# Kernel optimization log

Hardware: AMD Instinct MI355X
Metric: run time of the kernel (lower is better)

## Reference

```python
import jax, jax.numpy as jnp
import numpy as np

STRIDE = 14
C_LOCAL = 2
NUM_HEADS = 12


def sparse_attention_mask(n_tokens, stride_length=STRIDE, c=C_LOCAL, mode='fixed'):
    q = jnp.arange(n_tokens)[:, None]  # row index Q
    k = jnp.arange(n_tokens)[None, :]  # col index K
    if mode == 'fixed':
        m1 = (q // stride_length) == (k // stride_length)
        m2 = ((k % stride_length) >= stride_length - c) & ((k % stride_length) <= stride_length)
        return m1 | m2
    elif mode == 'strided':
        m1 = jnp.abs(q - k) <= stride_length
        m2 = ((q - k) % stride_length) == 0
        return m1 | m2


def setup_inputs() -> dict:
    key = jax.random.key(0)
    ks = jax.random.split(key, 5)
    B, N, C = 16, 1024, 768
    return {
        'x': jax.random.normal(ks[0], (B, N, C), dtype=jnp.float32),
        'w_qkv': jax.random.normal(ks[1], (3 * C, C), dtype=jnp.float32) * (1.0 / np.sqrt(C)),
        'b_qkv': jax.random.normal(ks[2], (3 * C,), dtype=jnp.float32) * 0.02,
        'w_proj': jax.random.normal(ks[3], (C, C), dtype=jnp.float32) * (1.0 / np.sqrt(C)),
        'b_proj': jax.random.normal(ks[4], (C,), dtype=jnp.float32) * 0.02,
    }


def reference(x, w_qkv, b_qkv, w_proj, b_proj):
    B, N, C = x.shape
    H = NUM_HEADS
    D = C // H
    mask = sparse_attention_mask(N, mode='fixed')  # [N, N] bool

    # qkv projection: [B,N,3C] -> [3,B,H,N,D]
    qkv = x @ w_qkv.T + b_qkv
    qkv = qkv.reshape(B, N, 3, H, D).transpose(2, 0, 3, 1, 4)
    q, k, v = qkv[0], qkv[1], qkv[2]

    # SDPA with default scale = 1/sqrt(head_dim) and boolean attn_mask
    scale = 1.0 / jnp.sqrt(jnp.asarray(D, dtype=x.dtype))
    scores = jnp.einsum('bhnd,bhmd->bhnm', q, k) * scale
    scores = jnp.where(mask[None, None, :, :], scores, jnp.finfo(scores.dtype).min)
    attn = jax.nn.softmax(scores, axis=-1)
    out = jnp.einsum('bhnm,bhmd->bhnd', attn, v)

    # merge heads and output projection
    out = out.transpose(0, 2, 1, 3).reshape(B, N, C)
    return out @ w_proj.T + b_proj
```

## Files before the change

kernel.cpp:

```cpp
#include <hip/hip_runtime.h>
#include <stdint.h>

typedef unsigned short u16;
typedef __attribute__((ext_vector_type(8))) short bf16x8;
typedef __attribute__((ext_vector_type(4))) short s16x4;
typedef __attribute__((ext_vector_type(4))) float f32x4;

__device__ __forceinline__ u16 f2bf(float f) {
  uint32_t x = __builtin_bit_cast(uint32_t, f);
  uint32_t r = (x + 0x7fffu + ((x >> 16) & 1u)) >> 16;
  return (u16)r;
}
__device__ __forceinline__ float bf2f(u16 u) {
  return __builtin_bit_cast(float, (uint32_t)u << 16);
}

typedef __attribute__((address_space(3))) uint32_t lds_u32;
typedef const __attribute__((address_space(1))) uint32_t glb_u32;
__device__ __forceinline__ void gload_lds16(const void* g, void* l) {
  __builtin_amdgcn_global_load_lds(
      reinterpret_cast<glb_u32*>(reinterpret_cast<uintptr_t>(g)),
      reinterpret_cast<lds_u32*>(reinterpret_cast<uintptr_t>(l)),
      16, 0, 0);
}

__global__ void cvt_split_kernel(const float* __restrict__ in, u16* __restrict__ hi,
                                 u16* __restrict__ lo, int n4) {
  typedef __attribute__((ext_vector_type(4))) float float4v;
  int i = blockIdx.x * 256 + threadIdx.x;
  const int stride = gridDim.x * 256;
  for (; i < n4; i += stride) {
    float4v v = *(const float4v*)(in + (size_t)i * 4);
    s16x4 hv;
#pragma unroll
    for (int j = 0; j < 4; ++j) hv[j] = (short)f2bf(v[j]);
    *(s16x4*)(hi + (size_t)i * 4) = hv;
    if (lo) {
      s16x4 lv;
#pragma unroll
      for (int j = 0; j < 4; ++j) lv[j] = (short)f2bf(v[j] - bf2f((u16)hv[j]));
      *(s16x4*)(lo + (size_t)i * 4) = lv;
    }
  }
}

template <int OUTF32>
__global__ __launch_bounds__(256, 2) void gemm_bt(
    const u16* __restrict__ A, const u16* __restrict__ B0,
    const float* __restrict__ bias, float* __restrict__ outF, u16* __restrict__ outB,
    int Ndim, int Kdim) {
  __shared__ u16 sA[128 * 32];
  __shared__ u16 sB0[128 * 32];

  const int tid = threadIdx.x;
  const int lane = tid & 63;
  const int wr = (tid >> 6) >> 1;
  const int wc = (tid >> 6) & 1;
  const int brow = blockIdx.x * 128;
  const int bcol = blockIdx.y * 128;

  f32x4 acc[4][4] = {};

  for (int k0 = 0; k0 < Kdim; k0 += 32) {
    __syncthreads();
#pragma unroll
    for (int j = 0; j < 2; ++j) {
      const int c = j * 256 + tid;
      const int row = c >> 2;
      const int off = (c & 3) * 8;
      gload_lds16(A + (size_t)(brow + row) * Kdim + k0 + off, &sA[c * 8]);
      gload_lds16(B0 + (size_t)(bcol + row) * Kdim + k0 + off, &sB0[c * 8]);
    }
    __syncthreads();

    bf16x8 a[4], b[4];
#pragma unroll
    for (int m = 0; m < 4; ++m)
      a[m] = *(const bf16x8*)&sA[(wr * 64 + m * 16 + (lane & 15)) * 32 + (lane >> 4) * 8];
#pragma unroll
    for (int n = 0; n < 4; ++n)
      b[n] = *(const bf16x8*)&sB0[(wc * 64 + n * 16 + (lane & 15)) * 32 + (lane >> 4) * 8];
#pragma unroll
    for (int m = 0; m < 4; ++m)
#pragma unroll
      for (int n = 0; n < 4; ++n)
        acc[m][n] = __builtin_amdgcn_mfma_f32_16x16x32_bf16(a[m], b[n], acc[m][n], 0, 0, 0);
  }

  const int r0 = (lane >> 4) * 4;
  const int cn = lane & 15;
#pragma unroll
  for (int n = 0; n < 4; ++n) {
    const int colg = bcol + wc * 64 + n * 16 + cn;
    const float bv = bias[colg];
#pragma unroll
    for (int m = 0; m < 4; ++m) {
      const int rowg = brow + wr * 64 + m * 16 + r0;
#pragma unroll
      for (int r = 0; r < 4; ++r) {
        const float v = acc[m][n][r] + bv;
        if (OUTF32)
          outF[(size_t)(rowg + r) * Ndim + colg] = v;
        else
          outB[(size_t)(rowg + r) * Ndim + colg] = f2bf(v);
      }
    }
  }
}

__global__ __launch_bounds__(256) void transpose_v_kernel(const u16* __restrict__ qkv,
                                                          u16* __restrict__ vt) {
  __shared__ u16 t[64][72];
  const int tid = threadIdx.x;
  const int nt = blockIdx.x, h = blockIdx.y, b = blockIdx.z;
  const u16* src = qkv + (size_t)(b * 1024 + nt * 64) * 2304 + 1536 + h * 64;
#pragma unroll
  for (int j = 0; j < 2; ++j) {
    const int c = j * 256 + tid;
    const int row = c >> 3;
    const int off = (c & 7) * 8;
    *(bf16x8*)&t[row][off] = *(const bf16x8*)(src + (size_t)row * 2304 + off);
  }
  __syncthreads();
  u16* dst = vt + (size_t)(b * 12 + h) * 64 * 1024 + nt * 64;
#pragma unroll
  for (int j = 0; j < 2; ++j) {
    const int c = j * 256 + tid;
    const int drow = c >> 3;
    const int noff = (c & 7) * 8;
    bf16x8 o;
#pragma unroll
    for (int i = 0; i < 8; ++i) o[i] = (short)t[noff + i][drow];
    *(bf16x8*)(dst + (size_t)drow * 1024 + noff) = o;
  }
}

__global__ __launch_bounds__(256) void gather_global_kernel(const u16* __restrict__ qkv,
                                                            u16* __restrict__ kgc,
                                                            u16* __restrict__ vgc) {
  __shared__ u16 tl[192][72];
  const int tid = threadIdx.x;
  const int h = blockIdx.x % 12;
  const int b = blockIdx.x / 12;
  const u16* Kg = qkv + (size_t)(b * 1024) * 2304 + 768 + h * 64;
  const u16* Vg = qkv + (size_t)(b * 1024) * 2304 + 1536 + h * 64;
  u16* kout = kgc + (size_t)blockIdx.x * 192 * 64;
  u16* vout = vgc + (size_t)blockIdx.x * 64 * 192;

  for (int t = tid; t < 1536; t += 256) {
    const int s = t >> 3, ch = t & 7;
    bf16x8 kv = {}, vv = {};
    if (s < 146) {
      const int tok = (s >> 1) * 14 + 12 + (s & 1);
      kv = *(const bf16x8*)(Kg + (size_t)tok * 2304 + ch * 8);
      vv = *(const bf16x8*)(Vg + (size_t)tok * 2304 + ch * 8);
    }
    *(bf16x8*)(kout + s * 64 + ch * 8) = kv;
    *(bf16x8*)&tl[s][ch * 8] = vv;
  }
  __syncthreads();
  for (int t = tid; t < 64 * 24; t += 256) {
    const int d = t / 24, c8 = (t % 24) * 8;
    bf16x8 o;
#pragma unroll
    for (int i = 0; i < 8; ++i) o[i] = (short)tl[c8 + i][d];
    *(bf16x8*)(vout + (size_t)d * 192 + c8) = o;
  }
}

__global__ __launch_bounds__(256, 2) void attn_kernel(const u16* __restrict__ qkv,
                                                      const u16* __restrict__ vt,
                                                      const u16* __restrict__ kgc,
                                                      const u16* __restrict__ vgc,
                                                      u16* __restrict__ ao) {
  __shared__ u16 sQ[64 * 64];
  __shared__ u16 sK[64 * 64];
  __shared__ u16 sV[64 * 64];
  __shared__ u16 sP[4][16 * 72];

  const int tid = threadIdx.x;
  const int lane = tid & 63;
  const int wid = tid >> 6;
  const int qt = blockIdx.x, h = blockIdx.y, b = blockIdx.z;
  const int q0 = qt * 64;
  const int colL = lane & 15;
  const int kgrp = lane >> 4;
  const int bh = b * 12 + h;

  const u16* Qg = qkv + (size_t)(b * 1024 + q0) * 2304 + h * 64;
  const u16* Kg = qkv + (size_t)(b * 1024) * 2304 + 768 + h * 64;
  const u16* Vt = vt + (size_t)bh * 64 * 1024;
  const u16* Kc = kgc + (size_t)bh * 192 * 64;
  const u16* Vc = vgc + (size_t)bh * 64 * 192;

  const int first_blk = q0 / 14;
  const int tok0a = (first_blk * 14) & ~7;

#pragma unroll
  for (int j = 0; j < 2; ++j) {
    const int c = j * 256 + tid;
    const int row = c >> 3;
    const int off = (c & 7) * 8;
    gload_lds16(Qg + (size_t)row * 2304 + off, &sQ[c * 8]);
  }
  __syncthreads();

  bf16x8 qf[2];
#pragma unroll
  for (int ks = 0; ks < 2; ++ks)
    qf[ks] = *(const bf16x8*)&sQ[(wid * 16 + colL) * 64 + ks * 32 + kgrp * 8];

  int qblk[4];
#pragma unroll
  for (int r = 0; r < 4; ++r) qblk[r] = (q0 + wid * 16 + kgrp * 4 + r) / 14;

  const float SCL = 0.125f * 1.44269504088896f;
  const float NEG = -3e38f;
  float mrun[4] = {NEG, NEG, NEG, NEG};
  float lsum[4] = {0.f, 0.f, 0.f, 0.f};
  f32x4 oacc[4] = {};

  for (int it = 0; it < 5; ++it) {
    __syncthreads();
    if (it < 3) {
#pragma unroll
      for (int j = 0; j < 2; ++j) {
        const int c = j * 256 + tid;
        const int row = c >> 3;
        const int sb = ((c & 7) * 16) ^ ((row & 7) << 4);
        gload_lds16((const char*)(Kc + (size_t)(it * 64 + row) * 64) + sb, &sK[c * 8]);
        gload_lds16((const char*)(Vc + (size_t)row * 192 + it * 64) + sb, &sV[c * 8]);
      }
    } else {
      const int tc0 = tok0a + (it - 3) * 64;
#pragma unroll
      for (int j = 0; j < 2; ++j) {
        const int c = j * 256 + tid;
        const int row = c >> 3;
        const int sb = ((c & 7) * 16) ^ ((row & 7) << 4);
        const int ktok = min(tc0 + row, 1023);
        gload_lds16((const char*)(Kg + (size_t)ktok * 2304) + sb, &sK[c * 8]);
        const int vb = min(tc0 * 2 + sb, 2032);
        gload_lds16((const char*)(Vt + (size_t)row * 1024) + vb, &sV[c * 8]);
      }
    }
    __syncthreads();

    f32x4 s[4] = {};
#pragma unroll
    for (int n = 0; n < 4; ++n) {
      const int row = n * 16 + colL;
#pragma unroll
      for (int ks = 0; ks < 2; ++ks) {
        const int cb = (ks * 32 + kgrp * 8) * 2;
        bf16x8 kf = *(const bf16x8*)((const char*)sK + row * 128 + (cb ^ ((row & 7) << 4)));
        s[n] = __builtin_amdgcn_mfma_f32_16x16x32_bf16(qf[ks], kf, s[n], 0, 0, 0);
      }
    }

    float sv[4][4];
    if (it < 3) {
#pragma unroll
      for (int n = 0; n < 4; ++n) {
        const bool gv = (it * 64 + n * 16 + colL) < 146;
#pragma unroll
        for (int r = 0; r < 4; ++r) sv[n][r] = gv ? s[n][r] * SCL : NEG;
      }
    } else {
      const int tc0 = tok0a + (it - 3) * 64;
#pragma unroll
      for (int n = 0; n < 4; ++n) {
        const int t = tc0 + n * 16 + colL;
        const int tb = t / 14;
        const bool cv = (t < 1024) && ((t - tb * 14) < 12);
#pragma unroll
        for (int r = 0; r < 4; ++r) {
          const bool ok = cv && (tb == qblk[r]);
          sv[n][r] = ok ? s[n][r] * SCL : NEG;
        }
      }
    }

    float pmax[4];
#pragma unroll
    for (int r = 0; r < 4; ++r) {
      float v = fmaxf(fmaxf(sv[0][r], sv[1][r]), fmaxf(sv[2][r], sv[3][r]));
#pragma unroll
      for (int msk = 1; msk <= 8; msk <<= 1) v = fmaxf(v, __shfl_xor(v, msk));
      pmax[r] = v;
    }

    float corr[4], psum[4];
#pragma unroll
    for (int r = 0; r < 4; ++r) {
      const float mn = fmaxf(mrun[r], pmax[r]);
      corr[r] = exp2f(mrun[r] - mn);
      mrun[r] = mn;
      psum[r] = 0.f;
    }

    float p[4][4];
#pragma unroll
    for (int n = 0; n < 4; ++n)
#pragma unroll
      for (int r = 0; r < 4; ++r) {
        p[n][r] = exp2f(sv[n][r] - mrun[r]);
        psum[r] += p[n][r];
      }

#pragma unroll
    for (int r = 0; r < 4; ++r) {
      float v = psum[r];
#pragma unroll
      for (int msk = 1; msk <= 8; msk <<= 1) v += __shfl_xor(v, msk);
      lsum[r] = lsum[r] * corr[r] + v;
    }

#pragma unroll
    for (int n = 0; n < 4; ++n)
#pragma unroll
      for (int r = 0; r < 4; ++r)
        sP[wid][(kgrp * 4 + r) * 72 + n * 16 + colL] = f2bf(p[n][r]);

#pragma unroll
    for (int dn = 0; dn < 4; ++dn)
#pragma unroll
      for (int r = 0; r < 4; ++r) oacc[dn][r] *= corr[r];

#pragma unroll
    for (int ks = 0; ks < 2; ++ks) {
      bf16x8 pf = *(const bf16x8*)&sP[wid][colL * 72 + ks * 32 + kgrp * 8];
#pragma unroll
      for (int dn = 0; dn < 4; ++dn) {
        const int vrow = dn * 16 + colL;
        const int cb = (ks * 32 + kgrp * 8) * 2;
        bf16x8 vf = *(const bf16x8*)((const char*)sV + vrow * 128 + (cb ^ ((vrow & 7) << 4)));
        oacc[dn] = __builtin_amdgcn_mfma_f32_16x16x32_bf16(pf, vf, oacc[dn], 0, 0, 0);
      }
    }
  }

  float inv[4];
#pragma unroll
  for (int r = 0; r < 4; ++r) inv[r] = 1.0f / lsum[r];
#pragma unroll
  for (int dn = 0; dn < 4; ++dn)
#pragma unroll
    for (int r = 0; r < 4; ++r) {
      const int rowg = b * 1024 + q0 + wid * 16 + kgrp * 4 + r;
      const int colg = h * 64 + dn * 16 + colL;
      ao[(size_t)rowg * 768 + colg] = f2bf(oacc[dn][r] * inv[r]);
    }
}

extern "C" void kernel_launch(void* const* d_in, const int* in_sizes, int n_in,
                              void* d_out, int out_size, void* d_ws, size_t ws_size,
                              hipStream_t stream) {
  const float* x = (const float*)d_in[0];
  const float* w_qkv = (const float*)d_in[1];
  const float* b_qkv = (const float*)d_in[2];
  const float* w_proj = (const float*)d_in[3];
  const float* b_proj = (const float*)d_in[4];
  float* out = (float*)d_out;

  char* ws = (char*)d_ws;
  size_t off = 0;
  auto alloc = [&](size_t bytes) {
    char* p = ws + off;
    off += (bytes + 255) & ~(size_t)255;
    return p;
  };
  u16* x_bf = (u16*)alloc(16384ull * 768 * 2);
  u16* wq_bf = (u16*)alloc(2304ull * 768 * 2);
  u16* wp_bf = (u16*)alloc(768ull * 768 * 2);
  u16* qkvb = (u16*)alloc(16384ull * 2304 * 2);
  u16* vt = (u16*)alloc(192ull * 64 * 1024 * 2);
  u16* kgc = (u16*)alloc(192ull * 192 * 64 * 2);
  u16* vgc = (u16*)alloc(192ull * 64 * 192 * 2);
  u16* ao = x_bf;

  cvt_split_kernel<<<dim3(4096), dim3(256), 0, stream>>>(x, x_bf, nullptr, 16384 * 768 / 4);
  cvt_split_kernel<<<dim3(1728), dim3(256), 0, stream>>>(w_qkv, wq_bf, nullptr, 2304 * 768 / 4);
  cvt_split_kernel<<<dim3(576), dim3(256), 0, stream>>>(w_proj, wp_bf, nullptr, 768 * 768 / 4);

  gemm_bt<0><<<dim3(128, 18), dim3(256), 0, stream>>>(x_bf, wq_bf, b_qkv,
                                                      nullptr, qkvb, 2304, 768);
  transpose_v_kernel<<<dim3(16, 12, 16), dim3(256), 0, stream>>>(qkvb, vt);
  gather_global_kernel<<<dim3(192), dim3(256), 0, stream>>>(qkvb, kgc, vgc);
  attn_kernel<<<dim3(16, 12, 16), dim3(256), 0, stream>>>(qkvb, vt, kgc, vgc, ao);
  gemm_bt<1><<<dim3(128, 6), dim3(256), 0, stream>>>(ao, wp_bf, b_proj,
                                                     out, nullptr, 768, 768);
}
```

Before: 203.0 us.

## Double-buffer LDS tiles in GEMM and attention kernels to overlap loads with MFMA

Both the bf16 GEMM and the sparse attention kernel now keep two LDS buffers for their streamed operand tiles (A/B in the GEMM, K/V in attention). Each loop iteration issues the async global-to-LDS load for the next tile before computing on the current one, and there is one barrier per iteration instead of two. The goal is to hide global memory latency behind the matrix-core work. In exchange, shared memory per block doubles for these tiles, which could limit occupancy, and the overlap only pays off if the compiler does not wait for the prefetch too early.

```diff
diff --git a/kernel.cpp b/kernel.cpp
--- a/kernel.cpp
+++ b/kernel.cpp
@@ -49,8 +49,8 @@
     const u16* __restrict__ A, const u16* __restrict__ B0,
     const float* __restrict__ bias, float* __restrict__ outF, u16* __restrict__ outB,
     int Ndim, int Kdim) {
-  __shared__ u16 sA[128 * 32];
-  __shared__ u16 sB0[128 * 32];
+  __shared__ u16 sA[2][128 * 32];
+  __shared__ u16 sB[2][128 * 32];
 
   const int tid = threadIdx.x;
   const int lane = tid & 63;
@@ -59,32 +59,41 @@
   const int brow = blockIdx.x * 128;
   const int bcol = blockIdx.y * 128;
 
-  f32x4 acc[4][4] = {};
-
-  for (int k0 = 0; k0 < Kdim; k0 += 32) {
-    __syncthreads();
+  auto stage = [&](int buf, int k0) {
 #pragma unroll
     for (int j = 0; j < 2; ++j) {
       const int c = j * 256 + tid;
-      const int row = c >> 2;
+      const int r = c >> 2;
       const int off = (c & 3) * 8;
-      gload_lds16(A + (size_t)(brow + row) * Kdim + k0 + off, &sA[c * 8]);
-      gload_lds16(B0 + (size_t)(bcol + row) * Kdim + k0 + off, &sB0[c * 8]);
-    }
-    __syncthreads();
+      gload_lds16(A + (size_t)(brow + r) * Kdim + k0 + off, &sA[buf][c * 8]);
+      gload_lds16(B0 + (size_t)(bcol + r) * Kdim + k0 + off, &sB[buf][c * 8]);
+    }
+  };
+
+  f32x4 acc[4][4] = {};
+
+  stage(0, 0);
+  __syncthreads();
+
+  const int nt = Kdim >> 5;
+  for (int t = 0; t < nt; ++t) {
+    const int cur = t & 1;
+    if (t + 1 < nt) stage(cur ^ 1, (t + 1) << 5);
 
     bf16x8 a[4], b[4];
 #pragma unroll
     for (int m = 0; m < 4; ++m)
-      a[m] = *(const bf16x8*)&sA[(wr * 64 + m * 16 + (lane & 15)) * 32 + (lane >> 4) * 8];
+      a[m] = *(const bf16x8*)&sA[cur][(wr * 64 + m * 16 + (lane & 15)) * 32 + (lane >> 4) * 8];
 #pragma unroll
     for (int n = 0; n < 4; ++n)
-      b[n] = *(const bf16x8*)&sB0[(wc * 64 + n * 16 + (lane & 15)) * 32 + (lane >> 4) * 8];
+      b[n] = *(const bf16x8*)&sB[cur][(wc * 64 + n * 16 + (lane & 15)) * 32 + (lane >> 4) * 8];
 #pragma unroll
     for (int m = 0; m < 4; ++m)
 #pragma unroll
       for (int n = 0; n < 4; ++n)
         acc[m][n] = __builtin_amdgcn_mfma_f32_16x16x32_bf16(a[m], b[n], acc[m][n], 0, 0, 0);
+
+    __syncthreads();
   }
 
   const int r0 = (lane >> 4) * 4;
@@ -174,8 +183,8 @@
                                                       const u16* __restrict__ vgc,
                                                       u16* __restrict__ ao) {
   __shared__ u16 sQ[64 * 64];
-  __shared__ u16 sK[64 * 64];
-  __shared__ u16 sV[64 * 64];
+  __shared__ u16 sK[2][64 * 64];
+  __shared__ u16 sV[2][64 * 64];
   __shared__ u16 sP[4][16 * 72];
 
   const int tid = threadIdx.x;
@@ -196,6 +205,31 @@
   const int first_blk = q0 / 14;
   const int tok0a = (first_blk * 14) & ~7;
 
+  auto stage_kv = [&](int buf, int it) {
+    if (it < 3) {
+#pragma unroll
+      for (int j = 0; j < 2; ++j) {
+        const int c = j * 256 + tid;
+        const int row = c >> 3;
+        const int sb = ((c & 7) * 16) ^ ((row & 7) << 4);
+        gload_lds16((const char*)(Kc + (size_t)(it * 64 + row) * 64) + sb, &sK[buf][c * 8]);
+        gload_lds16((const char*)(Vc + (size_t)row * 192 + it * 64) + sb, &sV[buf][c * 8]);
+      }
+    } else {
+      const int tc0 = tok0a + (it - 3) * 64;
+#pragma unroll
+      for (int j = 0; j < 2; ++j) {
+        const int c = j * 256 + tid;
+        const int row = c >> 3;
+        const int sb = ((c & 7) * 16) ^ ((row & 7) << 4);
+        const int ktok = min(tc0 + row, 1023);
+        gload_lds16((const char*)(Kg + (size_t)ktok * 2304) + sb, &sK[buf][c * 8]);
+        const int vb = min(tc0 * 2 + sb, 2032);
+        gload_lds16((const char*)(Vt + (size_t)row * 1024) + vb, &sV[buf][c * 8]);
+      }
+    }
+  };
+
 #pragma unroll
   for (int j = 0; j < 2; ++j) {
     const int c = j * 256 + tid;
@@ -203,6 +237,7 @@
     const int off = (c & 7) * 8;
     gload_lds16(Qg + (size_t)row * 2304 + off, &sQ[c * 8]);
   }
+  stage_kv(0, 0);
   __syncthreads();
 
   bf16x8 qf[2];
@@ -221,30 +256,8 @@
   f32x4 oacc[4] = {};
 
   for (int it = 0; it < 5; ++it) {
-    __syncthreads();
-    if (it < 3) {
-#pragma unroll
-      for (int j = 0; j < 2; ++j) {
-        const int c = j * 256 + tid;
-        const int row = c >> 3;
-        const int sb = ((c & 7) * 16) ^ ((row & 7) << 4);
-        gload_lds16((const char*)(Kc + (size_t)(it * 64 + row) * 64) + sb, &sK[c * 8]);
-        gload_lds16((const char*)(Vc + (size_t)row * 192 + it * 64) + sb, &sV[c * 8]);
-      }
-    } else {
-      const int tc0 = tok0a + (it - 3) * 64;
-#pragma unroll
-      for (int j = 0; j < 2; ++j) {
-        const int c = j * 256 + tid;
-        const int row = c >> 3;
-        const int sb = ((c & 7) * 16) ^ ((row & 7) << 4);
-        const int ktok = min(tc0 + row, 1023);
-        gload_lds16((const char*)(Kg + (size_t)ktok * 2304) + sb, &sK[c * 8]);
-        const int vb = min(tc0 * 2 + sb, 2032);
-        gload_lds16((const char*)(Vt + (size_t)row * 1024) + vb, &sV[c * 8]);
-      }
-    }
-    __syncthreads();
+    const int cur = it & 1;
+    if (it + 1 < 5) stage_kv(cur ^ 1, it + 1);
 
     f32x4 s[4] = {};
 #pragma unroll
@@ -253,7 +266,7 @@
 #pragma unroll
       for (int ks = 0; ks < 2; ++ks) {
         const int cb = (ks * 32 + kgrp * 8) * 2;
-        bf16x8 kf = *(const bf16x8*)((const char*)sK + row * 128 + (cb ^ ((row & 7) << 4)));
+        bf16x8 kf = *(const bf16x8*)((const char*)&sK[cur][0] + row * 128 + (cb ^ ((row & 7) << 4)));
         s[n] = __builtin_amdgcn_mfma_f32_16x16x32_bf16(qf[ks], kf, s[n], 0, 0, 0);
       }
     }
@@ -334,10 +347,12 @@
       for (int dn = 0; dn < 4; ++dn) {
         const int vrow = dn * 16 + colL;
         const int cb = (ks * 32 + kgrp * 8) * 2;
-        bf16x8 vf = *(const bf16x8*)((const char*)sV + vrow * 128 + (cb ^ ((vrow & 7) << 4)));
+        bf16x8 vf = *(const bf16x8*)((const char*)&sV[cur][0] + vrow * 128 + (cb ^ ((vrow & 7) << 4)));
         oacc[dn] = __builtin_amdgcn_mfma_f32_16x16x32_bf16(pf, vf, oacc[dn], 0, 0, 0);
       }
     }
+
+    __syncthreads();
   }
 
   float inv[4];
```

After: 200.6 us. No clear change (-1.1%).
